# Performance work log

Measured on AMD Instinct MI355X. Metric: run time of the kernel, lower is better.

## Reference

```python
import jax, jax.numpy as jnp
import numpy as np

B, DZ, DY, DX = 2, 200, 200, 100   # batch, voxel grid
N = 200000                          # active input voxels
C_IN, C_MID, C_OUT = 16, 64, 32
K = 27                              # 3x3x3 kernel offsets
EPS = 1e-5


def _pad_per_k(kid, a_in, a_out, pad_in, pad_out):
    # pack ragged per-offset pair lists into dense [K, Pmax] with dummy padding
    counts = np.bincount(kid, minlength=K)
    P = int(counts.max())
    I = np.full((K, P), pad_in, np.int32)
    O = np.full((K, P), pad_out, np.int32)
    order = np.argsort(kid, kind='stable')
    ks = kid[order]
    starts = np.cumsum(counts) - counts
    pos = np.arange(kid.size) - starts[ks]
    I[ks, pos] = a_in[order]
    O[ks, pos] = a_out[order]
    return I, O


def _build_structure(seed=0):
    # spconv-style indice-pair generation (rulebook) in numpy
    rng = np.random.default_rng(seed)
    lin = rng.choice(B * DZ * DY * DX, size=N, replace=False)
    b, r = np.divmod(lin, DZ * DY * DX)
    z, r = np.divmod(r, DY * DX)
    y, x = np.divmod(r, DX)
    coords = np.stack([b, z, y, x], 1)
    offs = np.stack(np.meshgrid(*[np.arange(3)] * 3, indexing='ij'), -1).reshape(K, 3)
    od = np.array([(DZ - 3) // 2 + 1, (DY - 3) // 2 + 1, (DX - 3) // 2 + 1])
    # stage 1: SparseConv3d k=3 s=2 p=0 -> output site o iff i = 2*o + k
    oc = coords[:, None, 1:] - offs[None]            # (N, 27, 3)
    valid = (oc >= 0).all(-1) & (oc % 2 == 0).all(-1)
    oq = oc // 2
    valid &= (oq < od).all(-1)
    pi, pk = np.nonzero(valid)
    oz, oy, ox = oq[pi, pk, 0], oq[pi, pk, 1], oq[pi, pk, 2]
    olin = ((coords[pi, 0] * od[0] + oz) * od[1] + oy) * od[2] + ox
    uniq, inv = np.unique(olin, return_inverse=True)
    n1 = int(len(uniq))
    p1_in, p1_out = _pad_per_k(pk, pi.astype(np.int32), inv.astype(np.int32), N, n1)
    # stage 2: SubMConv3d k=3 on stage-1 sites (output sites == input sites)
    c1b, r = np.divmod(uniq, od[0] * od[1] * od[2])
    c1z, r = np.divmod(r, od[1] * od[2])
    c1y, c1x = np.divmod(r, od[2])
    coords1 = np.stack([c1b, c1z, c1y, c1x], 1)
    nc = coords1[:, None, 1:] + (offs - 1)[None]     # (n1, 27, 3) neighbor coords
    valid2 = (nc >= 0).all(-1) & (nc < od).all(-1)
    pj, pk2 = np.nonzero(valid2)
    nl = ((coords1[pj, 0] * od[0] + nc[pj, pk2, 0]) * od[1] + nc[pj, pk2, 1]) * od[2] + nc[pj, pk2, 2]
    pos = np.minimum(np.searchsorted(uniq, nl), n1 - 1)
    ok = uniq[pos] == nl
    p2_in, p2_out = _pad_per_k(pk2[ok], pos[ok].astype(np.int32), pj[ok].astype(np.int32), n1, n1)
    return p1_in, p1_out, p2_in, p2_out, n1


def _ggs(feats, W, pin, pout, n_out):
    # gather-gemm-scatter sparse conv; pin padded with feats.shape[0], pout with n_out
    fpad = jnp.concatenate([feats, jnp.zeros((1, feats.shape[1]), feats.dtype)], 0)
    out = jnp.zeros((n_out + 1, W.shape[2]), feats.dtype)
    for k in range(W.shape[0]):
        out = out.at[pout[k]].add(fpad[pin[k]] @ W[k])
    return out[:n_out]


def _bn_relu(x, g, b):
    # BatchNorm1d (training-mode batch stats, biased var) + ReLU
    m = x.mean(0)
    v = x.var(0)
    return jax.nn.relu((x - m) * jax.lax.rsqrt(v + EPS) * g + b)


def setup_inputs():
    p1_in, p1_out, p2_in, p2_out, n1 = _build_structure(0)
    key = jax.random.key(0)
    k1, k2, k3, k4 = jax.random.split(key, 4)
    return {
        'feats': jax.random.normal(k1, (N, C_IN), jnp.float32),
        'W1': jax.random.normal(k2, (K, C_IN, C_MID), jnp.float32) * 0.05,
        'gamma1': jnp.ones((C_MID,), jnp.float32),
        'beta1': jnp.zeros((C_MID,), jnp.float32),
        'W2': jax.random.normal(k3, (K, C_MID, C_MID), jnp.float32) * 0.05,
        'gamma2': jnp.ones((C_MID,), jnp.float32),
        'beta2': jnp.zeros((C_MID,), jnp.float32),
        'W3': jax.random.normal(k4, (K, C_MID, C_OUT), jnp.float32) * 0.05,
        'p1_in': jnp.asarray(p1_in), 'p1_out': jnp.asarray(p1_out),
        'p2_in': jnp.asarray(p2_in), 'p2_out': jnp.asarray(p2_out),
        'n1': n1,
    }


def reference(feats, W1, gamma1, beta1, W2, gamma2, beta2, W3, p1_in, p1_out, p2_in, p2_out, n1):
    x = _ggs(feats, W1, p1_in, p1_out, n1)                        # SparseConv3d(Cin,64,3,2)
    x = _bn_relu(x, gamma1, beta1)
    x = _bn_relu(_ggs(x, W2, p2_in, p2_out, n1), gamma2, beta2)   # SubMConv3d(64,64,3)
    return _ggs(x, W3, p1_out, p1_in, N)                          # SparseInverseConv3d: pairs swapped
```

## Files before the change

### kernel.cpp

```cpp
#include <hip/hip_runtime.h>
#include <hip/hip_bf16.h>

typedef __bf16 bf16x8 __attribute__((ext_vector_type(8)));
typedef float f32x4 __attribute__((ext_vector_type(4)));

__device__ __forceinline__ unsigned short f2bf(float x) {
  union { float f; unsigned int u; } v; v.f = x;
  unsigned int r = (v.u + 0x7FFFu + ((v.u >> 16) & 1u)) >> 16;
  return (unsigned short)r;
}
__device__ __forceinline__ float bf2f(unsigned short u) {
  union { unsigned int u; float f; } v; v.u = ((unsigned int)u) << 16;
  return v.f;
}

__global__ void cvt_feats_kernel(const float* __restrict__ f, unsigned short* __restrict__ fb, int n16) {
  int t = blockIdx.x * 256 + threadIdx.x;
  if (t >= n16) return;
  int i = t >> 4, j = t & 15;
  fb[(size_t)i * 32 + j] = f2bf(f[t]);
}

__global__ void pack_w_kernel(const float* __restrict__ W, unsigned short* __restrict__ Wp,
                              int CI, int CO, int NT, int KK) {
  int t = blockIdx.x * 256 + threadIdx.x;
  int total = 27 * NT * KK * 512;
  if (t >= total) return;
  int j = t & 7, l = (t >> 3) & 63;
  int g = t >> 9;
  int kk = g % KK; g /= KK;
  int nt = g % NT; int k = g / NT;
  int kg = kk * 32 + ((l >> 4) * 8) + j;
  int c = nt * 16 + (l & 15);
  float v = (kg < CI) ? W[((size_t)k * CI + kg) * CO + c] : 0.0f;
  Wp[t] = f2bf(v);
}

__global__ void build_table_kernel(const int* __restrict__ pin, const int* __restrict__ pout,
                                   int P, int maxo, int* __restrict__ tab,
                                   const int* __restrict__ n_ptr, int n_cap) {
  int p = blockIdx.x * 256 + threadIdx.x;
  if (p >= P) return;
  int k = blockIdx.y;
  int n = n_cap;
  if (n_ptr) { int nv = n_ptr[0]; if (nv < n) n = nv; }
  size_t e = (size_t)k * P + p;
  int o = pout[e];
  if (o < n) tab[(size_t)k * maxo + o] = pin[e];
}

#define LDTAB(KC_, TARR) do {                                                    \
    int _kc = (KC_) > 26 ? 26 : (KC_);                                           \
    _Pragma("unroll") for (int _m = 0; _m < MT; ++_m)                            \
      TARR[_m] = tab[(size_t)_kc * maxo + rowm[_m]];                             \
  } while (0)

#define ISSUE_A(AB, TARR, D) do {                                                \
    if (SKIP) {                                                                  \
      bool _anyv = (TARR[0] >= 0);                                               \
      _Pragma("unroll") for (int _m = 1; _m < MT; ++_m)                          \
        _anyv = _anyv || (TARR[_m] >= 0);                                        \
      D = (__ballot(_anyv) != 0ull);                                             \
    }                                                                            \
    _Pragma("unroll") for (int _m = 0; _m < MT; ++_m) {                          \
      const unsigned short* _s = Xb + (size_t)(TARR[_m] < 0 ? zrow : TARR[_m]) * ROWS + lg * 8; \
      _Pragma("unroll") for (int kk = 0; kk < KK; ++kk)                          \
        AB[_m][kk] = *reinterpret_cast<const bf16x8*>(_s + kk * 32);             \
    }                                                                            \
  } while (0)

#define STAGE_B2(KB, PB) do {                                                    \
    _Pragma("unroll") for (int _s = 0; _s < 2; ++_s) {                           \
      if ((KB) + _s <= 26) {                                                     \
        size_t _kb = (size_t)((KB) + _s) * (size_t)SZ;                           \
        _Pragma("unroll") for (int _j = 0; _j < PER; ++_j) {                     \
          int _c = w * PER + _j;                                                 \
          const unsigned char* _gp = WpB + _kb + (size_t)_c * 1024 + (size_t)l * 16; \
          __builtin_amdgcn_global_load_lds(                                      \
              (const __attribute__((address_space(1))) void*)_gp,                \
              (__attribute__((address_space(3))) void*)((PB) + _s * SZ + _c * 1024), 16, 0, 0); \
        }                                                                        \
      }                                                                          \
    }                                                                            \
  } while (0)

#define STEP_CORE(BCUR, AB, D) do {                                              \
    if (!SKIP || (D)) {                                                          \
      _Pragma("unroll") for (int kk = 0; kk < KK; ++kk)                          \
        _Pragma("unroll") for (int nt = 0; nt < NT; ++nt) {                      \
          bf16x8 b = *reinterpret_cast<const bf16x8*>(&(BCUR)[(nt * KK + kk) * 1024 + l * 16]); \
          _Pragma("unroll") for (int _m = 0; _m < MT; ++_m)                      \
            acc[_m][nt] = __builtin_amdgcn_mfma_f32_16x16x32_bf16(AB[_m][kk], b, acc[_m][nt], 0, 0, 0); \
        }                                                                        \
    }                                                                            \
  } while (0)

#define GROUP_BARRIER() do {                                                     \
    __builtin_amdgcn_sched_barrier(0);                                           \
    asm volatile("s_waitcnt vmcnt(%0)" :: "n"(NWAIT) : "memory");                \
    __builtin_amdgcn_sched_barrier(0);                                           \
    __builtin_amdgcn_s_barrier();                                                \
  } while (0)

template<int KK, int NT, int MT, bool SKIP>
__global__ __launch_bounds__(256, 4) void conv_mfma_kernel(
    const unsigned short* __restrict__ Xb, const unsigned short* __restrict__ Wp,
    const int* __restrict__ tab, int maxo, int zrow,
    const int* __restrict__ n_ptr, int n_cap,
    unsigned short* __restrict__ outb, float* __restrict__ outf) {
  const int CO = NT * 16;
  const int ROWS = KK * 32;
  const int RPW = 16 * MT;
  constexpr int PER = (KK * NT) / 4;
  constexpr int SZ = KK * NT * 1024;
  constexpr int NWAIT = 2 * MT * KK + 2 * MT;

  __shared__ __align__(16) unsigned char Blds[2][2][SZ];

  int bid = blockIdx.x;
  {
    int nwg = gridDim.x;
    int q = nwg >> 3, r = nwg & 7;
    int xcd = bid & 7, orig = bid >> 3;
    bid = (xcd < r ? xcd * (q + 1) : r * (q + 1) + (xcd - r) * q) + orig;
  }

  int w = threadIdx.x >> 6, l = threadIdx.x & 63;
  int n_rows = n_cap;
  if (n_ptr) { int nv = n_ptr[0]; if (nv < n_rows) n_rows = nv; }
  if (bid * 4 * RPW >= n_rows) return;
  int lr = l & 15, lg = l >> 4;
  int wbase = bid * 4 * RPW + w * RPW;

  int rowm[MT];
#pragma unroll
  for (int m = 0; m < MT; ++m) {
    int r = wbase + m * 16 + lr;
    rowm[m] = r < n_rows ? r : (n_rows - 1);
  }

  const unsigned char* WpB = (const unsigned char*)Wp;

  f32x4 acc[MT][NT] = {};
  bf16x8 a0[MT][KK], a1[MT][KK];
  int tE[MT], tO[MT];
  bool dE = true, dO = true;

  LDTAB(0, tE);
  LDTAB(1, tO);
  STAGE_B2(0, &Blds[0][0][0]);
  __builtin_amdgcn_sched_barrier(0);
  ISSUE_A(a0, tE, dE);
  ISSUE_A(a1, tO, dO);
  LDTAB(2, tE);
  LDTAB(3, tO);
  GROUP_BARRIER();

#pragma unroll 1
  for (int g = 0; g < 13; ++g) {
    int kb = g * 2;
    unsigned char* bc = &Blds[g & 1][0][0];
    unsigned char* bn = &Blds[(g + 1) & 1][0][0];
    STAGE_B2(kb + 2, bn);
    __builtin_amdgcn_sched_barrier(0);
    STEP_CORE(bc + 0 * SZ, a0, dE); ISSUE_A(a0, tE, dE); LDTAB(kb + 4, tE);
    STEP_CORE(bc + 1 * SZ, a1, dO); ISSUE_A(a1, tO, dO); LDTAB(kb + 5, tO);
    GROUP_BARRIER();
  }
  STEP_CORE(&Blds[1][0][0], a0, dE);

#pragma unroll
  for (int mt = 0; mt < MT; ++mt) {
    int r0 = wbase + mt * 16 + lg * 4;
#pragma unroll
    for (int rr = 0; rr < 4; ++rr) {
      int row = r0 + rr;
      if (row < n_rows) {
#pragma unroll
        for (int nt = 0; nt < NT; ++nt) {
          size_t off = (size_t)row * CO + nt * 16 + lr;
          if (outf) outf[off] = acc[mt][nt][rr];
          else outb[off] = f2bf(acc[mt][nt][rr]);
        }
      }
    }
  }
}

__global__ void bn_stats_kernel(const unsigned short* __restrict__ xb,
                                const int* __restrict__ n_ptr, int n_cap,
                                float* __restrict__ stats) {
  int c = threadIdx.x & 63, q = threadIdx.x >> 6;
  int n = n_ptr[0]; if (n > n_cap) n = n_cap;
  float s = 0.f, ss = 0.f;
  for (int r = blockIdx.x * 4 + q; r < n; r += gridDim.x * 4) {
    float v = bf2f(xb[(size_t)r * 64 + c]);
    s += v; ss += v * v;
  }
  __shared__ float ls[8][64];
  ls[q][c] = s; ls[4 + q][c] = ss;
  __syncthreads();
  if (q == 0) {
    s = ls[0][c] + ls[1][c] + ls[2][c] + ls[3][c];
    ss = ls[4][c] + ls[5][c] + ls[6][c] + ls[7][c];
    atomicAdd(&stats[c], s);
    atomicAdd(&stats[64 + c], ss);
  }
}

__global__ void bn_apply_kernel(unsigned short* __restrict__ xb,
                                const int* __restrict__ n_ptr, int n_cap,
                                const float* __restrict__ stats,
                                const float* __restrict__ gamma, const float* __restrict__ beta) {
  int c = threadIdx.x & 63, q = threadIdx.x >> 6;
  int n = n_ptr[0]; if (n > n_cap) n = n_cap;
  float inv_n = 1.f / (float)n;
  float m = stats[c] * inv_n;
  float var = stats[64 + c] * inv_n - m * m;
  float sc = gamma[c] * rsqrtf(var + 1e-5f);
  float sh = beta[c] - m * sc;
  for (int r = blockIdx.x * 4 + q; r < n; r += gridDim.x * 4) {
    size_t off = (size_t)r * 64 + c;
    float v = bf2f(xb[off]) * sc + sh;
    xb[off] = f2bf(v > 0.f ? v : 0.f);
  }
}

extern "C" void kernel_launch(void* const* d_in, const int* in_sizes, int n_in,
                              void* d_out, int out_size, void* d_ws, size_t ws_size,
                              hipStream_t stream) {
  const float* feats  = (const float*)d_in[0];
  const float* W1     = (const float*)d_in[1];
  const float* g1     = (const float*)d_in[2];
  const float* b1     = (const float*)d_in[3];
  const float* W2     = (const float*)d_in[4];
  const float* g2     = (const float*)d_in[5];
  const float* b2     = (const float*)d_in[6];
  const float* W3     = (const float*)d_in[7];
  const int* p1_in    = (const int*)d_in[8];
  const int* p1_out   = (const int*)d_in[9];
  const int* p2_in    = (const int*)d_in[10];
  const int* p2_out   = (const int*)d_in[11];
  const int* d_n1     = (const int*)d_in[12];
  float* out = (float*)d_out;

  const int N  = in_sizes[0] / 16;
  const int P1 = in_sizes[8] / 27;
  const int P2 = in_sizes[10] / 27;
  long KP1 = in_sizes[8];
  int n1b = (int)(KP1 < 980100 ? KP1 : 980100);
  int maxo = n1b > N ? n1b : N;

  char* p = (char*)d_ws;
  auto alloc = [&](size_t bytes) -> char* {
    char* r = p; p += (bytes + 255) & ~(size_t)255; return r;
  };
  unsigned short* featsb = (unsigned short*)alloc((size_t)(N + 1) * 32 * 2);
  unsigned short* x1b    = (unsigned short*)alloc((size_t)(n1b + 1) * 64 * 2);
  unsigned short* x2b    = (unsigned short*)alloc((size_t)(n1b + 1) * 64 * 2);
  unsigned short* W1p    = (unsigned short*)alloc((size_t)27 * 4 * 1 * 512 * 2);
  unsigned short* W2p    = (unsigned short*)alloc((size_t)27 * 4 * 2 * 512 * 2);
  unsigned short* W3p    = (unsigned short*)alloc((size_t)27 * 2 * 2 * 512 * 2);
  int*   tab   = (int*)alloc((size_t)maxo * 27 * 4);
  float* stats = (float*)alloc(256 * 4);
  if ((size_t)(p - (char*)d_ws) > ws_size) return;

  hipMemsetAsync(featsb, 0, (size_t)(N + 1) * 32 * 2, stream);
  hipMemsetAsync(x1b + (size_t)n1b * 64, 0, 64 * 2, stream);
  hipMemsetAsync(x2b + (size_t)n1b * 64, 0, 64 * 2, stream);
  hipMemsetAsync(stats, 0, 256 * 4, stream);

  cvt_feats_kernel<<<(N * 16 + 255) / 256, 256, 0, stream>>>(feats, featsb, N * 16);
  pack_w_kernel<<<(27 * 4 * 1 * 512 + 255) / 256, 256, 0, stream>>>(W1, W1p, 16, 64, 4, 1);
  pack_w_kernel<<<(27 * 4 * 2 * 512 + 255) / 256, 256, 0, stream>>>(W2, W2p, 64, 64, 4, 2);
  pack_w_kernel<<<(27 * 2 * 2 * 512 + 255) / 256, 256, 0, stream>>>(W3, W3p, 64, 32, 2, 2);

  hipMemsetAsync(tab, 0xFF, (size_t)n1b * 27 * 4, stream);
  build_table_kernel<<<dim3((P1 + 255) / 256, 27), 256, 0, stream>>>(
      p1_in, p1_out, P1, n1b, tab, d_n1, n1b);
  conv_mfma_kernel<1, 4, 2, true><<<(n1b + 127) / 128, 256, 0, stream>>>(
      featsb, W1p, tab, n1b, N, d_n1, n1b, x1b, nullptr);
  bn_stats_kernel<<<1024, 256, 0, stream>>>(x1b, d_n1, n1b, stats);
  bn_apply_kernel<<<2048, 256, 0, stream>>>(x1b, d_n1, n1b, stats, g1, b1);

  hipMemsetAsync(tab, 0xFF, (size_t)n1b * 27 * 4, stream);
  build_table_kernel<<<dim3((P2 + 255) / 256, 27), 256, 0, stream>>>(
      p2_in, p2_out, P2, n1b, tab, d_n1, n1b);
  conv_mfma_kernel<2, 4, 2, false><<<(n1b + 127) / 128, 256, 0, stream>>>(
      x1b, W2p, tab, n1b, n1b, d_n1, n1b, x2b, nullptr);
  bn_stats_kernel<<<1024, 256, 0, stream>>>(x2b, d_n1, n1b, stats + 128);
  bn_apply_kernel<<<2048, 256, 0, stream>>>(x2b, d_n1, n1b, stats + 128, g2, b2);

  hipMemsetAsync(tab, 0xFF, (size_t)N * 27 * 4, stream);
  build_table_kernel<<<dim3((P1 + 255) / 256, 27), 256, 0, stream>>>(
      p1_out, p1_in, P1, N, tab, nullptr, N);
  conv_mfma_kernel<2, 2, 2, true><<<(N + 127) / 128, 256, 0, stream>>>(
      x2b, W3p, tab, N, n1b, nullptr, N, nullptr, out);
}
```

Measured before the change: 661.5 us.

## Pack two kernel offsets per MFMA K-slice in first sparse conv stage

```diff
diff --git a/kernel.cpp b/kernel.cpp
--- a/kernel.cpp
+++ b/kernel.cpp
@@ -17,8 +17,7 @@
 __global__ void cvt_feats_kernel(const float* __restrict__ f, unsigned short* __restrict__ fb, int n16) {
   int t = blockIdx.x * 256 + threadIdx.x;
   if (t >= n16) return;
-  int i = t >> 4, j = t & 15;
-  fb[(size_t)i * 32 + j] = f2bf(f[t]);
+  fb[t] = f2bf(f[t]);
 }
 
 __global__ void pack_w_kernel(const float* __restrict__ W, unsigned short* __restrict__ Wp,
@@ -36,6 +35,22 @@
   Wp[t] = f2bf(v);
 }
 
+__global__ void pack_w_paired_kernel(const float* __restrict__ W, unsigned short* __restrict__ Wp,
+                                     int CO, int NT) {
+  int t = blockIdx.x * 256 + threadIdx.x;
+  int total = 14 * NT * 512;
+  if (t >= total) return;
+  int j = t & 7, l = (t >> 3) & 63;
+  int g = t >> 9;
+  int nt = g % NT; int gp = g / NT;
+  int kg = ((l >> 4) * 8) + j;
+  int k = 2 * gp + (kg >= 16 ? 1 : 0);
+  int ci = kg & 15;
+  int c = nt * 16 + (l & 15);
+  float v = (k <= 26) ? W[((size_t)k * 16 + ci) * CO + c] : 0.0f;
+  Wp[t] = f2bf(v);
+}
+
 __global__ void build_table_kernel(const int* __restrict__ pin, const int* __restrict__ pout,
                                    int P, int maxo, int* __restrict__ tab,
                                    const int* __restrict__ n_ptr, int n_cap) {
@@ -50,9 +65,12 @@
 }
 
 #define LDTAB(KC_, TARR) do {                                                    \
-    int _kc = (KC_) > 26 ? 26 : (KC_);                                           \
-    _Pragma("unroll") for (int _m = 0; _m < MT; ++_m)                            \
-      TARR[_m] = tab[(size_t)_kc * maxo + rowm[_m]];                             \
+    int _k2 = PAIRED ? (2 * (KC_) + klb) : (KC_);                                \
+    int _kc = _k2 > 26 ? 26 : _k2;                                               \
+    _Pragma("unroll") for (int _m = 0; _m < MT; ++_m) {                          \
+      int _t = tab[(size_t)_kc * maxo + rowm[_m]];                               \
+      TARR[_m] = (PAIRED && _k2 > 26) ? -1 : _t;                                 \
+    }                                                                            \
   } while (0)
 
 #define ISSUE_A(AB, TARR, D) do {                                                \
@@ -63,7 +81,7 @@
       D = (__ballot(_anyv) != 0ull);                                             \
     }                                                                            \
     _Pragma("unroll") for (int _m = 0; _m < MT; ++_m) {                          \
-      const unsigned short* _s = Xb + (size_t)(TARR[_m] < 0 ? zrow : TARR[_m]) * ROWS + lg * 8; \
+      const unsigned short* _s = Xb + (size_t)(TARR[_m] < 0 ? zrow : TARR[_m]) * ROWS + loff; \
       _Pragma("unroll") for (int kk = 0; kk < KK; ++kk)                          \
         AB[_m][kk] = *reinterpret_cast<const bf16x8*>(_s + kk * 32);             \
     }                                                                            \
@@ -71,7 +89,7 @@
 
 #define STAGE_B2(KB, PB) do {                                                    \
     _Pragma("unroll") for (int _s = 0; _s < 2; ++_s) {                           \
-      if ((KB) + _s <= 26) {                                                     \
+      if ((KB) + _s <= MAXK) {                                                   \
         size_t _kb = (size_t)((KB) + _s) * (size_t)SZ;                           \
         _Pragma("unroll") for (int _j = 0; _j < PER; ++_j) {                     \
           int _c = w * PER + _j;                                                 \
@@ -102,17 +120,19 @@
     __builtin_amdgcn_s_barrier();                                                \
   } while (0)
 
-template<int KK, int NT, int MT, bool SKIP>
+template<int KK, int NT, int MT, bool SKIP, bool PAIRED>
 __global__ __launch_bounds__(256, 4) void conv_mfma_kernel(
     const unsigned short* __restrict__ Xb, const unsigned short* __restrict__ Wp,
     const int* __restrict__ tab, int maxo, int zrow,
     const int* __restrict__ n_ptr, int n_cap,
     unsigned short* __restrict__ outb, float* __restrict__ outf) {
   const int CO = NT * 16;
-  const int ROWS = KK * 32;
+  const int ROWS = PAIRED ? 16 : KK * 32;
   const int RPW = 16 * MT;
   constexpr int PER = (KK * NT) / 4;
   constexpr int SZ = KK * NT * 1024;
+  constexpr int MAXK = PAIRED ? 13 : 26;
+  constexpr int GROUPS = PAIRED ? 6 : 13;
   constexpr int NWAIT = 2 * MT * KK + 2 * MT;
 
   __shared__ __align__(16) unsigned char Blds[2][2][SZ];
@@ -130,6 +150,8 @@
   if (n_ptr) { int nv = n_ptr[0]; if (nv < n_rows) n_rows = nv; }
   if (bid * 4 * RPW >= n_rows) return;
   int lr = l & 15, lg = l >> 4;
+  int klb = lg >> 1;
+  int loff = PAIRED ? (lg & 1) * 8 : lg * 8;
   int wbase = bid * 4 * RPW + w * RPW;
 
   int rowm[MT];
@@ -157,7 +179,7 @@
   GROUP_BARRIER();
 
 #pragma unroll 1
-  for (int g = 0; g < 13; ++g) {
+  for (int g = 0; g < GROUPS; ++g) {
     int kb = g * 2;
     unsigned char* bc = &Blds[g & 1][0][0];
     unsigned char* bn = &Blds[(g + 1) & 1][0][0];
@@ -167,7 +189,11 @@
     STEP_CORE(bc + 1 * SZ, a1, dO); ISSUE_A(a1, tO, dO); LDTAB(kb + 5, tO);
     GROUP_BARRIER();
   }
-  STEP_CORE(&Blds[1][0][0], a0, dE);
+  {
+    unsigned char* bt = &Blds[GROUPS & 1][0][0];
+    STEP_CORE(bt + 0 * SZ, a0, dE);
+    if (PAIRED) STEP_CORE(bt + 1 * SZ, a1, dO);
+  }
 
 #pragma unroll
   for (int mt = 0; mt < MT; ++mt) {
@@ -255,30 +281,30 @@
   auto alloc = [&](size_t bytes) -> char* {
     char* r = p; p += (bytes + 255) & ~(size_t)255; return r;
   };
-  unsigned short* featsb = (unsigned short*)alloc((size_t)(N + 1) * 32 * 2);
+  unsigned short* featsb = (unsigned short*)alloc((size_t)(N + 1) * 16 * 2);
   unsigned short* x1b    = (unsigned short*)alloc((size_t)(n1b + 1) * 64 * 2);
   unsigned short* x2b    = (unsigned short*)alloc((size_t)(n1b + 1) * 64 * 2);
-  unsigned short* W1p    = (unsigned short*)alloc((size_t)27 * 4 * 1 * 512 * 2);
+  unsigned short* W1p    = (unsigned short*)alloc((size_t)14 * 4 * 512 * 2);
   unsigned short* W2p    = (unsigned short*)alloc((size_t)27 * 4 * 2 * 512 * 2);
   unsigned short* W3p    = (unsigned short*)alloc((size_t)27 * 2 * 2 * 512 * 2);
   int*   tab   = (int*)alloc((size_t)maxo * 27 * 4);
   float* stats = (float*)alloc(256 * 4);
   if ((size_t)(p - (char*)d_ws) > ws_size) return;
 
-  hipMemsetAsync(featsb, 0, (size_t)(N + 1) * 32 * 2, stream);
+  hipMemsetAsync(featsb + (size_t)N * 16, 0, 16 * 2, stream);
   hipMemsetAsync(x1b + (size_t)n1b * 64, 0, 64 * 2, stream);
   hipMemsetAsync(x2b + (size_t)n1b * 64, 0, 64 * 2, stream);
   hipMemsetAsync(stats, 0, 256 * 4, stream);
 
   cvt_feats_kernel<<<(N * 16 + 255) / 256, 256, 0, stream>>>(feats, featsb, N * 16);
-  pack_w_kernel<<<(27 * 4 * 1 * 512 + 255) / 256, 256, 0, stream>>>(W1, W1p, 16, 64, 4, 1);
+  pack_w_paired_kernel<<<(14 * 4 * 512 + 255) / 256, 256, 0, stream>>>(W1, W1p, 64, 4);
   pack_w_kernel<<<(27 * 4 * 2 * 512 + 255) / 256, 256, 0, stream>>>(W2, W2p, 64, 64, 4, 2);
   pack_w_kernel<<<(27 * 2 * 2 * 512 + 255) / 256, 256, 0, stream>>>(W3, W3p, 64, 32, 2, 2);
 
   hipMemsetAsync(tab, 0xFF, (size_t)n1b * 27 * 4, stream);
   build_table_kernel<<<dim3((P1 + 255) / 256, 27), 256, 0, stream>>>(
       p1_in, p1_out, P1, n1b, tab, d_n1, n1b);
-  conv_mfma_kernel<1, 4, 2, true><<<(n1b + 127) / 128, 256, 0, stream>>>(
+  conv_mfma_kernel<1, 4, 2, true, true><<<(n1b + 127) / 128, 256, 0, stream>>>(
       featsb, W1p, tab, n1b, N, d_n1, n1b, x1b, nullptr);
   bn_stats_kernel<<<1024, 256, 0, stream>>>(x1b, d_n1, n1b, stats);
   bn_apply_kernel<<<2048, 256, 0, stream>>>(x1b, d_n1, n1b, stats, g1, b1);
@@ -286,7 +312,7 @@
   hipMemsetAsync(tab, 0xFF, (size_t)n1b * 27 * 4, stream);
   build_table_kernel<<<dim3((P2 + 255) / 256, 27), 256, 0, stream>>>(
       p2_in, p2_out, P2, n1b, tab, d_n1, n1b);
-  conv_mfma_kernel<2, 4, 2, false><<<(n1b + 127) / 128, 256, 0, stream>>>(
+  conv_mfma_kernel<2, 4, 2, false, false><<<(n1b + 127) / 128, 256, 0, stream>>>(
       x1b, W2p, tab, n1b, n1b, d_n1, n1b, x2b, nullptr);
   bn_stats_kernel<<<1024, 256, 0, stream>>>(x2b, d_n1, n1b, stats + 128);
   bn_apply_kernel<<<2048, 256, 0, stream>>>(x2b, d_n1, n1b, stats + 128, g2, b2);
@@ -294,6 +320,6 @@
   hipMemsetAsync(tab, 0xFF, (size_t)N * 27 * 4, stream);
   build_table_kernel<<<dim3((P1 + 255) / 256, 27), 256, 0, stream>>>(
       p1_out, p1_in, P1, N, tab, nullptr, N);
-  conv_mfma_kernel<2, 2, 2, true><<<(N + 127) / 128, 256, 0, stream>>>(
+  conv_mfma_kernel<2, 2, 2, true, false><<<(N + 127) / 128, 256, 0, stream>>>(
       x2b, W3p, tab, N, n1b, nullptr, N, nullptr, out);
 }
```

Measured after the change: 634.2 us (median of 2 runs). 4.1% less time.
